# Performance work log

Hardware: AMD Instinct MI355X
Metric: run time of the kernel (lower is better)

The kernel has to match this reference:

```python
import jax, jax.numpy as jnp
import numpy as np

CH = [32, 64, 128, 256, 512]
# per decoder stage s (s=0 deepest): conv_a Cin = CH[3-s] + in_ch, Cout = CH[3-s]; conv_b CH[3-s]->CH[3-s]
STAGE_DIMS = [(768, 256), (384, 128), (192, 64), (96, 32)]


def three_interpolation(p1, p2, x2):
    """p1 [B,N1,3] dense coords, p2 [B,N2,3] sparse coords, x2 [B,C,N2] -> [B,C,N1]."""
    d2 = (jnp.sum(p1 * p1, -1)[:, :, None]
          - 2.0 * jnp.einsum('bnd,bmd->bnm', p1, p2)
          + jnp.sum(p2 * p2, -1)[:, None, :])            # [B,N1,N2] squared dists
    neg_d, idx = jax.lax.top_k(-d2, 3)                   # 3 nearest neighbors
    dist = jnp.maximum(-neg_d, 0.0)                      # [B,N1,3]
    w = 1.0 / (dist + 1e-8)
    w = w / jnp.sum(w, axis=-1, keepdims=True)           # inverse-distance weights
    gathered = jax.vmap(lambda x, i: x[:, i])(x2, idx)   # [B,C,N1,3]
    return jnp.einsum('bcnk,bnk->bcn', gathered, w)


def conv_bn_relu(x, W, g, b):
    # 1x1 conv1d + BN (eval: running mean 0, var 1) + ReLU
    y = jnp.einsum('oc,bcn->bon', W, x)
    return jax.nn.relu(y * g[None, :, None] + b[None, :, None])


def setup_inputs() -> dict:
    key = jax.random.key(0)
    B = 8
    Ns = [8192, 2048, 512, 128, 32]
    inp = {}
    keys = jax.random.split(key, 64)
    ki = 0
    for i, n in enumerate(Ns):
        inp[f'p{i}'] = jax.random.uniform(keys[ki], (B, n, 3), jnp.float32); ki += 1
        inp[f'f{i}'] = jax.random.normal(keys[ki], (B, CH[i], n), jnp.float32); ki += 1
    for s, (cin, cout) in enumerate(STAGE_DIMS):
        inp[f'w{s}a'] = jax.random.normal(keys[ki], (cout, cin), jnp.float32) * 0.05; ki += 1
        inp[f'g{s}a'] = 1.0 + 0.1 * jax.random.normal(keys[ki], (cout,), jnp.float32); ki += 1
        inp[f'b{s}a'] = 0.1 * jax.random.normal(keys[ki], (cout,), jnp.float32); ki += 1
        inp[f'w{s}b'] = jax.random.normal(keys[ki], (cout, cout), jnp.float32) * 0.05; ki += 1
        inp[f'g{s}b'] = 1.0 + 0.1 * jax.random.normal(keys[ki], (cout,), jnp.float32); ki += 1
        inp[f'b{s}b'] = 0.1 * jax.random.normal(keys[ki], (cout,), jnp.float32); ki += 1
    return inp


def reference(p0, p1, p2, p3, p4, f0, f1, f2, f3, f4,
              w0a, g0a, b0a, w0b, g0b, b0b,
              w1a, g1a, b1a, w1b, g1b, b1b,
              w2a, g2a, b2a, w2b, g2b, b2b,
              w3a, g3a, b3a, w3b, g3b, b3b):
    p = [p0, p1, p2, p3, p4]
    f = [f0, f1, f2, f3, f4]
    params = [(w0a, g0a, b0a, w0b, g0b, b0b),
              (w1a, g1a, b1a, w1b, g1b, b1b),
              (w2a, g2a, b2a, w2b, g2b, b2b),
              (w3a, g3a, b3a, w3b, g3b, b3b)]
    # decoder stage s propagates level (4-s) -> (3-s)
    for s in range(4):
        lvl = 3 - s
        interp = three_interpolation(p[lvl], p[lvl + 1], f[lvl + 1])
        x = jnp.concatenate([f[lvl], interp], axis=1)
        wa, ga, ba, wb, gb, bb = params[s]
        x = conv_bn_relu(x, wa, ga, ba)
        x = conv_bn_relu(x, wb, gb, bb)
        f[lvl] = x
    return f[0]
```

## Files before the change

kernel.cpp:

```cpp
#include <hip/hip_runtime.h>

#define KNN_INF 3.0e38f

struct KnnAll {
    const float* p1[4]; const float* p2[4];
    float* pd[4]; int* pi[4];
    int N1[4], N2[4], chunk[4], nchunk[4], nbx[4];
    int blkStart[4];
    int bs1, bs2, bs3;
};

__global__ void knn_all_kernel(KnnAll P) {
    __shared__ float4 sm4[256];
    int bid = blockIdx.x;
    int s = (bid >= P.bs1) + (bid >= P.bs2) + (bid >= P.bs3);
    int start = (s == 0) ? 0 : (s == 1) ? P.bs1 : (s == 2) ? P.bs2 : P.bs3;
    int local = bid - start;
    int nbx = P.nbx[s];
    int bx = local % nbx;
    int rest = local / nbx;
    int b = rest & 7;
    int z = rest >> 3;
    int N1 = P.N1[s], N2 = P.N2[s], chunk = P.chunk[s], nchunk = P.nchunk[s];
    int m0 = z * chunk;
    const float* p2b = P.p2[s] + ((size_t)b * N2 + m0) * 3;
    for (int m = threadIdx.x; m < chunk; m += blockDim.x) {
        float x = p2b[m * 3 + 0], y = p2b[m * 3 + 1], zz = p2b[m * 3 + 2];
        sm4[m] = make_float4(x, y, zz, x * x + y * y + zz * zz);
    }
    __syncthreads();
    int n = bx * blockDim.x + threadIdx.x;
    if (n >= N1) return;
    const float* p1b = P.p1[s] + ((size_t)b * N1 + n) * 3;
    float px = p1b[0], py = p1b[1], pz = p1b[2];
    float s1 = px * px + py * py + pz * pz;
    float d0 = KNN_INF, d1 = KNN_INF, d2 = KNN_INF;
    int i0 = 0, i1 = 0, i2 = 0;
    for (int m = 0; m < chunk; ++m) {
        float4 q = sm4[m];
        float dot = px * q.x + py * q.y + pz * q.z;
        float d = fmaf(-2.0f, dot, s1 + q.w);
        if (d < d2) {
            if (d < d1) {
                d2 = d1; i2 = i1;
                if (d < d0) { d1 = d0; i1 = i0; d0 = d; i0 = m; }
                else        { d1 = d;  i1 = m; }
            } else { d2 = d; i2 = m; }
        }
    }
    size_t base = (((size_t)b * N1 + n) * nchunk + z) * 3;
    float* pd = P.pd[s]; int* pi = P.pi[s];
    pd[base + 0] = d0; pd[base + 1] = d1; pd[base + 2] = d2;
    pi[base + 0] = m0 + i0; pi[base + 1] = m0 + i1; pi[base + 2] = m0 + i2;
}

struct MergeAll {
    const float* pd[4]; const int* pi[4];
    int* idx[4]; float* w[4];
    int nchunk[4], N1[4];
    int ts1, ts2, ts3;
};

__global__ void knn_merge_all_kernel(MergeAll P) {
    int t = blockIdx.x * blockDim.x + threadIdx.x;
    int s = (t >= P.ts1) + (t >= P.ts2) + (t >= P.ts3);
    int start = (s == 0) ? 0 : (s == 1) ? P.ts1 : (s == 2) ? P.ts2 : P.ts3;
    int lt = t - start;
    int nchunk = P.nchunk[s];
    float d0 = KNN_INF, d1 = KNN_INF, d2 = KNN_INF;
    int i0 = 0, i1 = 0, i2 = 0;
    const float* pd = P.pd[s]; const int* pi = P.pi[s];
    size_t base = (size_t)lt * nchunk * 3;
    for (int c = 0; c < nchunk * 3; ++c) {
        float d = pd[base + c];
        int   i = pi[base + c];
        if (d < d2) {
            if (d < d1) {
                d2 = d1; i2 = i1;
                if (d < d0) { d1 = d0; i1 = i0; d0 = d; i0 = i; }
                else        { d1 = d;  i1 = i; }
            } else { d2 = d; i2 = i; }
        }
    }
    float dd0 = fmaxf(d0, 0.0f), dd1 = fmaxf(d1, 0.0f), dd2 = fmaxf(d2, 0.0f);
    float w0 = 1.0f / (dd0 + 1e-8f);
    float w1 = 1.0f / (dd1 + 1e-8f);
    float w2 = 1.0f / (dd2 + 1e-8f);
    float wsum = w0 + w1 + w2;
    w0 /= wsum; w1 /= wsum; w2 /= wsum;
    size_t ob = (size_t)lt * 3;
    P.idx[s][ob + 0] = i0; P.idx[s][ob + 1] = i1; P.idx[s][ob + 2] = i2;
    P.w[s][ob + 0] = w0; P.w[s][ob + 1] = w1; P.w[s][ob + 2] = w2;
}

#define TO 32
#define TN 64
#define BK 16
template<bool PARTIAL>
__global__ __launch_bounds__(256) void conv_a_fused_kernel(
    const float* __restrict__ f1,
    const float* __restrict__ x2,
    const int*   __restrict__ idxS,
    const float* __restrict__ wS,
    const float* __restrict__ W,
    const float* __restrict__ g,
    const float* __restrict__ bv,
    float* __restrict__ Y,
    int C1, int C2, int N, int N2, int Cout, int chunk) {
    __shared__ float Ws[BK][TO];
    __shared__ float Xs[BK][TN];
    int Cin = C1 + C2;
    int zb = blockIdx.z;
    int b = zb & 7;
    int split = zb >> 3;
    int kBase = split * chunk;
    int oBase = blockIdx.y * TO;
    int nBase = blockIdx.x * TN;
    int tid = threadIdx.x;
    int tx = tid & 15;
    int ty = tid >> 4;
    int nn = tid & 63;
    int kk0 = tid >> 6;
    int n = nBase + nn;
    size_t gb = ((size_t)b * N + n) * 3;
    int j0 = idxS[gb + 0], j1 = idxS[gb + 1], j2 = idxS[gb + 2];
    float w0g = wS[gb + 0], w1g = wS[gb + 1], w2g = wS[gb + 2];
    const float* f1b = f1 + (size_t)b * C1 * N;
    const float* x2b = x2 + (size_t)b * C2 * N2;
    float acc[2][4] = {{0.f, 0.f, 0.f, 0.f}, {0.f, 0.f, 0.f, 0.f}};
    for (int k0 = kBase; k0 < kBase + chunk; k0 += BK) {
        for (int t = tid; t < TO * BK; t += 256) {
            int o = t / BK, kk = t % BK;
            Ws[kk][o] = W[(size_t)(oBase + o) * Cin + k0 + kk];
        }
#pragma unroll
        for (int i = 0; i < 4; ++i) {
            int kk = kk0 + i * 4;
            int k = k0 + kk;
            float v;
            if (k < C1) {
                v = f1b[(size_t)k * N + n];
            } else {
                const float* r = x2b + (size_t)(k - C1) * N2;
                v = r[j0] * w0g + r[j1] * w1g + r[j2] * w2g;
            }
            Xs[kk][nn] = v;
        }
        __syncthreads();
#pragma unroll
        for (int kk = 0; kk < BK; ++kk) {
            float w0 = Ws[kk][ty * 2 + 0];
            float w1 = Ws[kk][ty * 2 + 1];
            float4 xv = *reinterpret_cast<const float4*>(&Xs[kk][tx * 4]);
            acc[0][0] = fmaf(w0, xv.x, acc[0][0]);
            acc[0][1] = fmaf(w0, xv.y, acc[0][1]);
            acc[0][2] = fmaf(w0, xv.z, acc[0][2]);
            acc[0][3] = fmaf(w0, xv.w, acc[0][3]);
            acc[1][0] = fmaf(w1, xv.x, acc[1][0]);
            acc[1][1] = fmaf(w1, xv.y, acc[1][1]);
            acc[1][2] = fmaf(w1, xv.z, acc[1][2]);
            acc[1][3] = fmaf(w1, xv.w, acc[1][3]);
        }
        __syncthreads();
    }
#pragma unroll
    for (int r = 0; r < 2; ++r) {
        int o = oBase + ty * 2 + r;
        float4 st;
        if (PARTIAL) {
            st.x = acc[r][0]; st.y = acc[r][1]; st.z = acc[r][2]; st.w = acc[r][3];
            *reinterpret_cast<float4*>(&Y[((size_t)zb * Cout + o) * N + nBase + tx * 4]) = st;
        } else {
            float gg = g[o], bb = bv[o];
            st.x = fmaxf(fmaf(acc[r][0], gg, bb), 0.0f);
            st.y = fmaxf(fmaf(acc[r][1], gg, bb), 0.0f);
            st.z = fmaxf(fmaf(acc[r][2], gg, bb), 0.0f);
            st.w = fmaxf(fmaf(acc[r][3], gg, bb), 0.0f);
            *reinterpret_cast<float4*>(&Y[((size_t)b * Cout + o) * N + nBase + tx * 4]) = st;
        }
    }
}

template<bool PARTIAL>
__global__ __launch_bounds__(256) void conv_gemm_kernel(
    const float* __restrict__ X,
    const float* __restrict__ W,
    const float* __restrict__ g,
    const float* __restrict__ bv,
    float* __restrict__ Y,
    int Cin, int Cout, int N, int chunk) {
    __shared__ float Ws[BK][TO];
    __shared__ float Xs[BK][TN];
    int zb = blockIdx.z;
    int b = zb & 7;
    int split = zb >> 3;
    int kBase = split * chunk;
    int oBase = blockIdx.y * TO;
    int nBase = blockIdx.x * TN;
    int tid = threadIdx.x;
    int tx = tid & 15;
    int ty = tid >> 4;
    float acc[2][4] = {{0.f, 0.f, 0.f, 0.f}, {0.f, 0.f, 0.f, 0.f}};
    const float* Xb = X + (size_t)b * Cin * N;
    for (int k0 = kBase; k0 < kBase + chunk; k0 += BK) {
        for (int t = tid; t < TO * BK; t += 256) {
            int o = t / BK, kk = t % BK;
            Ws[kk][o] = W[(size_t)(oBase + o) * Cin + k0 + kk];
        }
        for (int t = tid; t < BK * TN; t += 256) {
            int kk = t / TN, nnn = t % TN;
            Xs[kk][nnn] = Xb[(size_t)(k0 + kk) * N + nBase + nnn];
        }
        __syncthreads();
#pragma unroll
        for (int kk = 0; kk < BK; ++kk) {
            float w0 = Ws[kk][ty * 2 + 0];
            float w1 = Ws[kk][ty * 2 + 1];
            float4 xv = *reinterpret_cast<const float4*>(&Xs[kk][tx * 4]);
            acc[0][0] = fmaf(w0, xv.x, acc[0][0]);
            acc[0][1] = fmaf(w0, xv.y, acc[0][1]);
            acc[0][2] = fmaf(w0, xv.z, acc[0][2]);
            acc[0][3] = fmaf(w0, xv.w, acc[0][3]);
            acc[1][0] = fmaf(w1, xv.x, acc[1][0]);
            acc[1][1] = fmaf(w1, xv.y, acc[1][1]);
            acc[1][2] = fmaf(w1, xv.z, acc[1][2]);
            acc[1][3] = fmaf(w1, xv.w, acc[1][3]);
        }
        __syncthreads();
    }
#pragma unroll
    for (int r = 0; r < 2; ++r) {
        int o = oBase + ty * 2 + r;
        float4 st;
        if (PARTIAL) {
            st.x = acc[r][0]; st.y = acc[r][1]; st.z = acc[r][2]; st.w = acc[r][3];
            *reinterpret_cast<float4*>(&Y[((size_t)zb * Cout + o) * N + nBase + tx * 4]) = st;
        } else {
            float gg = g[o], bb = bv[o];
            st.x = fmaxf(fmaf(acc[r][0], gg, bb), 0.0f);
            st.y = fmaxf(fmaf(acc[r][1], gg, bb), 0.0f);
            st.z = fmaxf(fmaf(acc[r][2], gg, bb), 0.0f);
            st.w = fmaxf(fmaf(acc[r][3], gg, bb), 0.0f);
            *reinterpret_cast<float4*>(&Y[((size_t)b * Cout + o) * N + nBase + tx * 4]) = st;
        }
    }
}

__global__ void reduce_bn_relu_kernel(const float* __restrict__ part,
                                      const float* __restrict__ g,
                                      const float* __restrict__ bv,
                                      float* __restrict__ Y,
                                      int Cout, int N, int total4, int nsplit, int stride4) {
    int t = blockIdx.x * blockDim.x + threadIdx.x;
    if (t >= total4) return;
    const float4* p4 = reinterpret_cast<const float4*>(part);
    float4 a = p4[t];
    for (int s = 1; s < nsplit; ++s) {
        float4 v = p4[t + (size_t)s * stride4];
        a.x += v.x; a.y += v.y; a.z += v.z; a.w += v.w;
    }
    int o = ((t * 4) / N) % Cout;
    float gg = g[o], bb = bv[o];
    float4 st;
    st.x = fmaxf(fmaf(a.x, gg, bb), 0.0f);
    st.y = fmaxf(fmaf(a.y, gg, bb), 0.0f);
    st.z = fmaxf(fmaf(a.z, gg, bb), 0.0f);
    st.w = fmaxf(fmaf(a.w, gg, bb), 0.0f);
    reinterpret_cast<float4*>(Y)[t] = st;
}

extern "C" void kernel_launch(void* const* d_in, const int* in_sizes, int n_in,
                              void* d_out, int out_size, void* d_ws, size_t ws_size,
                              hipStream_t stream) {
    const int B = 8;
    const int Ns[5]  = {8192, 2048, 512, 128, 32};
    const int CHs[5] = {32, 64, 128, 256, 512};

    const float* p[5];
    const float* f[5];
    for (int i = 0; i < 5; ++i) {
        p[i] = (const float*)d_in[2 * i];
        f[i] = (const float*)d_in[2 * i + 1];
    }

    int N1s[4], N2s[4], C1s[4], C2s[4];
    for (int s = 0; s < 4; ++s) {
        int lvl = 3 - s;
        N1s[s] = Ns[lvl]; N2s[s] = Ns[lvl + 1];
        C1s[s] = CHs[lvl];
        C2s[s] = (s == 0) ? CHs[4] : CHs[lvl + 1];
    }
    const int nchunks[4] = {1, 4, 8, 8};
    int chunks[4], nbxs[4];
    for (int s = 0; s < 4; ++s) {
        chunks[s] = N2s[s] / nchunks[s];
        nbxs[s] = (N1s[s] + 255) / 256;
    }

    float* ws = (float*)d_ws;
    int*   knn_idx = (int*)ws;
    float* knn_w   = ws + 262144;
    float* part_d  = ws + 524288;
    int*   part_i  = (int*)(ws + 2621440);
    float* bufA    = ws + 4718592;
    float* out0    = ws + 6815744;
    float* out1    = ws + 7077888;
    float* out2    = ws + 7602176;
    float* gpart   = ws + 8650752;
    float* outs[4] = {out0, out1, out2, (float*)d_out};

    int idxOff[4], pOff[4];
    {
        int a = 0, q = 0;
        for (int s = 0; s < 4; ++s) {
            idxOff[s] = a; a += B * N1s[s] * 3;
            pOff[s] = q;  q += B * N1s[s] * nchunks[s] * 3;
        }
    }

    KnnAll KP;
    int blk = 0;
    int bsArr[4];
    for (int s = 0; s < 4; ++s) {
        KP.p1[s] = p[3 - s]; KP.p2[s] = p[4 - s];
        KP.pd[s] = part_d + pOff[s]; KP.pi[s] = part_i + pOff[s];
        KP.N1[s] = N1s[s]; KP.N2[s] = N2s[s];
        KP.chunk[s] = chunks[s]; KP.nchunk[s] = nchunks[s]; KP.nbx[s] = nbxs[s];
        bsArr[s] = blk;
        blk += nbxs[s] * B * nchunks[s];
    }
    KP.bs1 = (blk, bsArr[1]); KP.bs2 = bsArr[2]; KP.bs3 = bsArr[3];
    knn_all_kernel<<<blk, 256, 0, stream>>>(KP);

    MergeAll MP;
    int tt = 0;
    int tsArr[4];
    for (int s = 0; s < 4; ++s) {
        MP.pd[s] = part_d + pOff[s]; MP.pi[s] = part_i + pOff[s];
        MP.idx[s] = knn_idx + idxOff[s]; MP.w[s] = knn_w + idxOff[s];
        MP.nchunk[s] = nchunks[s]; MP.N1[s] = N1s[s];
        tsArr[s] = tt;
        tt += B * N1s[s];
    }
    MP.ts1 = tsArr[1]; MP.ts2 = tsArr[2]; MP.ts3 = tsArr[3];
    knn_merge_all_kernel<<<(tt + 255) / 256, 256, 0, stream>>>(MP);

    const int nsA[4] = {6, 3, 2, 1};
    const int nsB[4] = {4, 2, 1, 1};

    for (int s = 0; s < 4; ++s) {
        int N1 = N1s[s], N2 = N2s[s];
        int C1 = C1s[s], C2 = C2s[s];
        int Cin = C1 + C2, Cout = C1;
        const float* x2 = (s == 0) ? f[4] : outs[s - 1];
        const float* wa = (const float*)d_in[10 + s * 6 + 0];
        const float* ga = (const float*)d_in[10 + s * 6 + 1];
        const float* ba = (const float*)d_in[10 + s * 6 + 2];
        const float* wb = (const float*)d_in[10 + s * 6 + 3];
        const float* gb = (const float*)d_in[10 + s * 6 + 4];
        const float* bb = (const float*)d_in[10 + s * 6 + 5];
        const int* idxS = knn_idx + idxOff[s];
        const float* wSb = knn_w + idxOff[s];

        {
            int nsplit = nsA[s];
            int chunk = Cin / nsplit;
            dim3 grid(N1 / TN, Cout / TO, B * nsplit);
            if (nsplit == 1) {
                conv_a_fused_kernel<false><<<grid, 256, 0, stream>>>(
                    f[3 - s], x2, idxS, wSb, wa, ga, ba, bufA, C1, C2, N1, N2, Cout, chunk);
            } else {
                conv_a_fused_kernel<true><<<grid, 256, 0, stream>>>(
                    f[3 - s], x2, idxS, wSb, wa, ga, ba, gpart, C1, C2, N1, N2, Cout, chunk);
                int total4 = B * Cout * N1 / 4;
                reduce_bn_relu_kernel<<<(total4 + 255) / 256, 256, 0, stream>>>(
                    gpart, ga, ba, bufA, Cout, N1, total4, nsplit, total4);
            }
        }
        {
            int nsplit = nsB[s];
            int chunk = Cout / nsplit;
            dim3 grid(N1 / TN, Cout / TO, B * nsplit);
            if (nsplit == 1) {
                conv_gemm_kernel<false><<<grid, 256, 0, stream>>>(
                    bufA, wb, gb, bb, outs[s], Cout, Cout, N1, chunk);
            } else {
                conv_gemm_kernel<true><<<grid, 256, 0, stream>>>(
                    bufA, wb, gb, bb, gpart, Cout, Cout, N1, chunk);
                int total4 = B * Cout * N1 / 4;
                reduce_bn_relu_kernel<<<(total4 + 255) / 256, 256, 0, stream>>>(
                    gpart, gb, bb, outs[s], Cout, N1, total4, nsplit, total4);
            }
        }
    }
}
```

Before: 231.5 us.

## Use uniform grid binning for last-stage KNN and increase split-K factors

Replaces the brute-force chunked 3-NN search for the largest stage (8192 queries vs 2048 points) with a per-batch uniform 8x8x8 grid: a binning kernel counting-sorts points into cells, and a query kernel scans neighbouring cells with an expanding ring and an early-exit bound. This removes most of the O(N1*N2) distance work and the partial/merge traffic for that stage. Ties are broken by original index to match top_k ordering. It also doubles the split-K factors for the conv GEMMs in the deeper stages to raise parallelism, at the cost of more partial-sum reduction traffic.

```diff
diff --git a/kernel.cpp b/kernel.cpp
--- a/kernel.cpp
+++ b/kernel.cpp
@@ -1,20 +1,163 @@
 #include <hip/hip_runtime.h>
 
 #define KNN_INF 3.0e38f
+#define GD 8
+#define NCELL 512
+#define H 0.125f
+
+
+__global__ __launch_bounds__(512) void bin_kernel(const float* __restrict__ p2,
+                                                  float4* __restrict__ bpts,
+                                                  int* __restrict__ bidx,
+                                                  int* __restrict__ cstart,
+                                                  int N2) {
+    __shared__ int cnt[NCELL], cnt0[NCELL], cur[NCELL];
+    __shared__ int cellof[2048];
+    int b = blockIdx.x;
+    int t = threadIdx.x;
+    cnt[t] = 0;
+    __syncthreads();
+    float xs[4], ys[4], zs[4];
+    for (int i = 0; i < 4; ++i) {
+        int m = t * 4 + i;
+        const float* q = p2 + ((size_t)b * N2 + m) * 3;
+        float x = q[0], y = q[1], z = q[2];
+        xs[i] = x; ys[i] = y; zs[i] = z;
+        int ix = min(GD - 1, max(0, (int)(x * 8.0f)));
+        int iy = min(GD - 1, max(0, (int)(y * 8.0f)));
+        int iz = min(GD - 1, max(0, (int)(z * 8.0f)));
+        int c = (ix << 6) | (iy << 3) | iz;
+        cellof[m] = c;
+        atomicAdd(&cnt[c], 1);
+    }
+    __syncthreads();
+    int myc = cnt[t];
+    cnt0[t] = myc;
+    __syncthreads();
+    for (int off = 1; off < NCELL; off <<= 1) {
+        int v = (t >= off) ? cnt[t - off] : 0;
+        __syncthreads();
+        cnt[t] += v;
+        __syncthreads();
+    }
+    int excl = cnt[t] - cnt0[t];
+    cur[t] = excl;
+    cstart[b * (NCELL + 1) + t] = excl;
+    if (t == 0) cstart[b * (NCELL + 1) + NCELL] = N2;
+    __syncthreads();
+    for (int i = 0; i < 4; ++i) {
+        int m = t * 4 + i;
+        int c = cellof[m];
+        int pos = atomicAdd(&cur[c], 1);
+        float x = xs[i], y = ys[i], z = zs[i];
+        bpts[(size_t)b * N2 + pos] = make_float4(x, y, z, x * x + y * y + z * z);
+        bidx[(size_t)b * N2 + pos] = m;
+    }
+}
+
+__device__ __forceinline__ bool lex_lt(float da, int ia, float db, int ib) {
+    return (da < db) || (da == db && ia < ib);
+}
+
+__global__ __launch_bounds__(256) void knn_query_kernel(
+    const float* __restrict__ p1,
+    const float4* __restrict__ bpts,
+    const int* __restrict__ bidx,
+    const int* __restrict__ cstart,
+    int* __restrict__ idx, float* __restrict__ w,
+    int N1, int N2) {
+    int n = blockIdx.x * 256 + threadIdx.x;
+    int b = blockIdx.y;
+    if (n >= N1) return;
+    const float* pp = p1 + ((size_t)b * N1 + n) * 3;
+    float px = pp[0], py = pp[1], pz = pp[2];
+    float s1 = px * px + py * py + pz * pz;
+    int cx = min(GD - 1, max(0, (int)(px * 8.0f)));
+    int cy = min(GD - 1, max(0, (int)(py * 8.0f)));
+    int cz = min(GD - 1, max(0, (int)(pz * 8.0f)));
+    float d0 = KNN_INF, d1 = KNN_INF, d2 = KNN_INF;
+    int i0 = 0, i1 = 0, i2 = 0;
+    const float4* bp = bpts + (size_t)b * N2;
+    const int* bi = bidx + (size_t)b * N2;
+    const int* cs = cstart + b * (NCELL + 1);
+
+#define SCAN_CELL(ci, cj, ck)                                            \
+    {                                                                    \
+        int c_ = ((ci) << 6) | ((cj) << 3) | (ck);                       \
+        int e_ = cs[c_ + 1];                                             \
+        for (int m_ = cs[c_]; m_ < e_; ++m_) {                           \
+            float4 q = bp[m_];                                           \
+            int om = bi[m_];                                             \
+            float dot = px * q.x + py * q.y + pz * q.z;                  \
+            float d = fmaf(-2.0f, dot, s1 + q.w);                        \
+            if (lex_lt(d, om, d2, i2)) {                                 \
+                if (lex_lt(d, om, d1, i1)) {                             \
+                    d2 = d1; i2 = i1;                                    \
+                    if (lex_lt(d, om, d0, i0)) {                         \
+                        d1 = d0; i1 = i0; d0 = d; i0 = om;               \
+                    } else { d1 = d; i1 = om; }                          \
+                } else { d2 = d; i2 = om; }                              \
+            }                                                            \
+        }                                                                \
+    }
+
+    int x0 = max(cx - 1, 0), x1 = min(cx + 1, GD - 1);
+    int y0 = max(cy - 1, 0), y1 = min(cy + 1, GD - 1);
+    int z0 = max(cz - 1, 0), z1 = min(cz + 1, GD - 1);
+    for (int i = x0; i <= x1; ++i)
+        for (int j = y0; j <= y1; ++j)
+            for (int k = z0; k <= z1; ++k)
+                SCAN_CELL(i, j, k);
+
+    int r = 1;
+    while (true) {
+        float mL = (cx - r > 0)      ? (px - (float)(cx - r) * H)     : KNN_INF;
+        float mR = (cx + r < GD - 1) ? ((float)(cx + r + 1) * H - px) : KNN_INF;
+        float mD = (cy - r > 0)      ? (py - (float)(cy - r) * H)     : KNN_INF;
+        float mU = (cy + r < GD - 1) ? ((float)(cy + r + 1) * H - py) : KNN_INF;
+        float mB = (cz - r > 0)      ? (pz - (float)(cz - r) * H)     : KNN_INF;
+        float mF = (cz + r < GD - 1) ? ((float)(cz + r + 1) * H - pz) : KNN_INF;
+        float mg = fminf(fminf(fminf(mL, mR), fminf(mD, mU)), fminf(mB, mF));
+        if (mg >= 1.0e18f) break;
+        if (d2 <= mg * mg * 0.99999f) break;
+        int nx0 = max(cx - r - 1, 0), nx1 = min(cx + r + 1, GD - 1);
+        int ny0 = max(cy - r - 1, 0), ny1 = min(cy + r + 1, GD - 1);
+        int nz0 = max(cz - r - 1, 0), nz1 = min(cz + r + 1, GD - 1);
+        for (int i = nx0; i <= nx1; ++i)
+            for (int j = ny0; j <= ny1; ++j)
+                for (int k = nz0; k <= nz1; ++k) {
+                    if (i >= x0 && i <= x1 && j >= y0 && j <= y1 && k >= z0 && k <= z1)
+                        continue;
+                    SCAN_CELL(i, j, k);
+                }
+        x0 = nx0; x1 = nx1; y0 = ny0; y1 = ny1; z0 = nz0; z1 = nz1;
+        ++r;
+    }
+#undef SCAN_CELL
+
+    float dd0 = fmaxf(d0, 0.0f), dd1 = fmaxf(d1, 0.0f), dd2 = fmaxf(d2, 0.0f);
+    float w0 = 1.0f / (dd0 + 1e-8f);
+    float w1 = 1.0f / (dd1 + 1e-8f);
+    float w2 = 1.0f / (dd2 + 1e-8f);
+    float wsum = w0 + w1 + w2;
+    w0 /= wsum; w1 /= wsum; w2 /= wsum;
+    size_t ob = ((size_t)b * N1 + n) * 3;
+    idx[ob + 0] = i0; idx[ob + 1] = i1; idx[ob + 2] = i2;
+    w[ob + 0] = w0; w[ob + 1] = w1; w[ob + 2] = w2;
+}
 
 struct KnnAll {
-    const float* p1[4]; const float* p2[4];
-    float* pd[4]; int* pi[4];
-    int N1[4], N2[4], chunk[4], nchunk[4], nbx[4];
-    int blkStart[4];
-    int bs1, bs2, bs3;
+    const float* p1[3]; const float* p2[3];
+    float* pd[3]; int* pi[3];
+    int N1[3], N2[3], chunk[3], nchunk[3], nbx[3];
+    int bs1, bs2;
 };
 
 __global__ void knn_all_kernel(KnnAll P) {
     __shared__ float4 sm4[256];
     int bid = blockIdx.x;
-    int s = (bid >= P.bs1) + (bid >= P.bs2) + (bid >= P.bs3);
-    int start = (s == 0) ? 0 : (s == 1) ? P.bs1 : (s == 2) ? P.bs2 : P.bs3;
+    int s = (bid >= P.bs1) + (bid >= P.bs2);
+    int start = (s == 0) ? 0 : (s == 1) ? P.bs1 : P.bs2;
     int local = bid - start;
     int nbx = P.nbx[s];
     int bx = local % nbx;
@@ -55,16 +198,17 @@
 }
 
 struct MergeAll {
-    const float* pd[4]; const int* pi[4];
-    int* idx[4]; float* w[4];
-    int nchunk[4], N1[4];
-    int ts1, ts2, ts3;
+    const float* pd[3]; const int* pi[3];
+    int* idx[3]; float* w[3];
+    int nchunk[3];
+    int ts1, ts2;
 };
 
-__global__ void knn_merge_all_kernel(MergeAll P) {
+__global__ void knn_merge_all_kernel(MergeAll P, int total) {
     int t = blockIdx.x * blockDim.x + threadIdx.x;
-    int s = (t >= P.ts1) + (t >= P.ts2) + (t >= P.ts3);
-    int start = (s == 0) ? 0 : (s == 1) ? P.ts1 : (s == 2) ? P.ts2 : P.ts3;
+    if (t >= total) return;
+    int s = (t >= P.ts1) + (t >= P.ts2);
+    int start = (s == 0) ? 0 : (s == 1) ? P.ts1 : P.ts2;
     int lt = t - start;
     int nchunk = P.nchunk[s];
     float d0 = KNN_INF, d1 = KNN_INF, d2 = KNN_INF;
@@ -98,13 +242,9 @@
 #define BK 16
 template<bool PARTIAL>
 __global__ __launch_bounds__(256) void conv_a_fused_kernel(
-    const float* __restrict__ f1,
-    const float* __restrict__ x2,
-    const int*   __restrict__ idxS,
-    const float* __restrict__ wS,
-    const float* __restrict__ W,
-    const float* __restrict__ g,
-    const float* __restrict__ bv,
+    const float* __restrict__ f1, const float* __restrict__ x2,
+    const int* __restrict__ idxS, const float* __restrict__ wS,
+    const float* __restrict__ W, const float* __restrict__ g, const float* __restrict__ bv,
     float* __restrict__ Y,
     int C1, int C2, int N, int N2, int Cout, int chunk) {
     __shared__ float Ws[BK][TO];
@@ -183,12 +323,9 @@
 
 template<bool PARTIAL>
 __global__ __launch_bounds__(256) void conv_gemm_kernel(
-    const float* __restrict__ X,
-    const float* __restrict__ W,
-    const float* __restrict__ g,
-    const float* __restrict__ bv,
-    float* __restrict__ Y,
-    int Cin, int Cout, int N, int chunk) {
+    const float* __restrict__ X, const float* __restrict__ W,
+    const float* __restrict__ g, const float* __restrict__ bv,
+    float* __restrict__ Y, int Cin, int Cout, int N, int chunk) {
     __shared__ float Ws[BK][TO];
     __shared__ float Xs[BK][TN];
     int zb = blockIdx.z;
@@ -290,9 +427,9 @@
         C1s[s] = CHs[lvl];
         C2s[s] = (s == 0) ? CHs[4] : CHs[lvl + 1];
     }
-    const int nchunks[4] = {1, 4, 8, 8};
-    int chunks[4], nbxs[4];
-    for (int s = 0; s < 4; ++s) {
+    const int nchunks[3] = {1, 4, 8};
+    int chunks[3], nbxs[3];
+    for (int s = 0; s < 3; ++s) {
         chunks[s] = N2s[s] / nchunks[s];
         nbxs[s] = (N1s[s] + 255) / 256;
     }
@@ -301,27 +438,37 @@
     int*   knn_idx = (int*)ws;
     float* knn_w   = ws + 262144;
     float* part_d  = ws + 524288;
-    int*   part_i  = (int*)(ws + 2621440);
-    float* bufA    = ws + 4718592;
-    float* out0    = ws + 6815744;
-    float* out1    = ws + 7077888;
-    float* out2    = ws + 7602176;
-    float* gpart   = ws + 8650752;
+    int*   part_i  = (int*)(ws + 969728);
+    float* bufA    = ws + 1415168;
+    float* out0    = ws + 3512320;
+    float* out1    = ws + 3774464;
+    float* out2    = ws + 4298752;
+    float* gpart   = ws + 5347328;
+    float4* bin_pts = (float4*)(ws + 9541632);
+    int*   bin_idx  = (int*)(ws + 9672704);
+    int*   cell_st  = (int*)(ws + 9689088);
     float* outs[4] = {out0, out1, out2, (float*)d_out};
 
-    int idxOff[4], pOff[4];
+    int idxOff[4], pOff[3];
     {
-        int a = 0, q = 0;
-        for (int s = 0; s < 4; ++s) {
-            idxOff[s] = a; a += B * N1s[s] * 3;
-            pOff[s] = q;  q += B * N1s[s] * nchunks[s] * 3;
-        }
+        int a = 0;
+        for (int s = 0; s < 4; ++s) { idxOff[s] = a; a += B * N1s[s] * 3; }
+        int q = 0;
+        for (int s = 0; s < 3; ++s) { pOff[s] = q; q += B * N1s[s] * nchunks[s] * 3; }
+    }
+
+    bin_kernel<<<B, 512, 0, stream>>>(p[1], bin_pts, bin_idx, cell_st, N2s[3]);
+    {
+        dim3 qg(N1s[3] / 256, B);
+        knn_query_kernel<<<qg, 256, 0, stream>>>(p[0], bin_pts, bin_idx, cell_st,
+                                                 knn_idx + idxOff[3], knn_w + idxOff[3],
+                                                 N1s[3], N2s[3]);
     }
 
     KnnAll KP;
     int blk = 0;
-    int bsArr[4];
-    for (int s = 0; s < 4; ++s) {
+    int bsArr[3];
+    for (int s = 0; s < 3; ++s) {
         KP.p1[s] = p[3 - s]; KP.p2[s] = p[4 - s];
         KP.pd[s] = part_d + pOff[s]; KP.pi[s] = part_i + pOff[s];
         KP.N1[s] = N1s[s]; KP.N2[s] = N2s[s];
@@ -329,24 +476,24 @@
         bsArr[s] = blk;
         blk += nbxs[s] * B * nchunks[s];
     }
-    KP.bs1 = (blk, bsArr[1]); KP.bs2 = bsArr[2]; KP.bs3 = bsArr[3];
+    KP.bs1 = bsArr[1]; KP.bs2 = bsArr[2];
     knn_all_kernel<<<blk, 256, 0, stream>>>(KP);
 
     MergeAll MP;
     int tt = 0;
-    int tsArr[4];
-    for (int s = 0; s < 4; ++s) {
+    int tsArr[3];
+    for (int s = 0; s < 3; ++s) {
         MP.pd[s] = part_d + pOff[s]; MP.pi[s] = part_i + pOff[s];
         MP.idx[s] = knn_idx + idxOff[s]; MP.w[s] = knn_w + idxOff[s];
-        MP.nchunk[s] = nchunks[s]; MP.N1[s] = N1s[s];
+        MP.nchunk[s] = nchunks[s];
         tsArr[s] = tt;
         tt += B * N1s[s];
     }
-    MP.ts1 = tsArr[1]; MP.ts2 = tsArr[2]; MP.ts3 = tsArr[3];
-    knn_merge_all_kernel<<<(tt + 255) / 256, 256, 0, stream>>>(MP);
-
-    const int nsA[4] = {6, 3, 2, 1};
-    const int nsB[4] = {4, 2, 1, 1};
+    MP.ts1 = tsArr[1]; MP.ts2 = tsArr[2];
+    knn_merge_all_kernel<<<(tt + 255) / 256, 256, 0, stream>>>(MP, tt);
+
+    const int nsA[4] = {12, 6, 4, 1};
+    const int nsB[4] = {8, 4, 2, 1};
 
     for (int s = 0; s < 4; ++s) {
         int N1 = N1s[s], N2 = N2s[s];
```

Result: slower. 271.5 us (+17.3%).

## Pre-pack sparse coords into float4 and read them directly in KNN scan

Applied to the files above, without the earlier changes.

Adds a pack kernel that converts the sparse point clouds into float4 (xyz plus squared norm) once. The KNN scan then reads these packed values straight from global memory (uniform, cached loads) instead of staging them in shared memory with a barrier. It also drops the per-point s1 add from the inner loop and adds it back only at the end. The merge kernel gains a bounds check and the workspace layout is reshuffled. This costs one extra launch and trades LDS reads for cached global reads in the hot loop.

```diff
diff --git a/kernel.cpp b/kernel.cpp
--- a/kernel.cpp
+++ b/kernel.cpp
@@ -2,16 +2,30 @@
 
 #define KNN_INF 3.0e38f
 
-struct KnnAll {
-    const float* p1[4]; const float* p2[4];
+struct PackAll {
+    const float* src[4];
+    float4* dst[4];
+    int c1, c2, c3;
+};
+__global__ void pack_kernel(PackAll P, int total) {
+    int t = blockIdx.x * 256 + threadIdx.x;
+    if (t >= total) return;
+    int s = (t >= P.c1) + (t >= P.c2) + (t >= P.c3);
+    int start = (s == 0) ? 0 : (s == 1) ? P.c1 : (s == 2) ? P.c2 : P.c3;
+    int i = t - start;
+    const float* q = P.src[s] + (size_t)i * 3;
+    float x = q[0], y = q[1], z = q[2];
+    P.dst[s][i] = make_float4(x, y, z, x * x + y * y + z * z);
+}
+
+struct KnnAll4 {
+    const float* p1[4];
+    const float4* c4[4];
     float* pd[4]; int* pi[4];
     int N1[4], N2[4], chunk[4], nchunk[4], nbx[4];
-    int blkStart[4];
     int bs1, bs2, bs3;
 };
-
-__global__ void knn_all_kernel(KnnAll P) {
-    __shared__ float4 sm4[256];
+__global__ __launch_bounds__(256) void knn_all_kernel(KnnAll4 P) {
     int bid = blockIdx.x;
     int s = (bid >= P.bs1) + (bid >= P.bs2) + (bid >= P.bs3);
     int start = (s == 0) ? 0 : (s == 1) ? P.bs1 : (s == 2) ? P.bs2 : P.bs3;
@@ -23,46 +37,41 @@
     int z = rest >> 3;
     int N1 = P.N1[s], N2 = P.N2[s], chunk = P.chunk[s], nchunk = P.nchunk[s];
     int m0 = z * chunk;
-    const float* p2b = P.p2[s] + ((size_t)b * N2 + m0) * 3;
-    for (int m = threadIdx.x; m < chunk; m += blockDim.x) {
-        float x = p2b[m * 3 + 0], y = p2b[m * 3 + 1], zz = p2b[m * 3 + 2];
-        sm4[m] = make_float4(x, y, zz, x * x + y * y + zz * zz);
-    }
-    __syncthreads();
-    int n = bx * blockDim.x + threadIdx.x;
+    const float4* __restrict__ cb = P.c4[s] + (size_t)b * N2 + m0;
+    int n = bx * 256 + threadIdx.x;
     if (n >= N1) return;
     const float* p1b = P.p1[s] + ((size_t)b * N1 + n) * 3;
     float px = p1b[0], py = p1b[1], pz = p1b[2];
     float s1 = px * px + py * py + pz * pz;
-    float d0 = KNN_INF, d1 = KNN_INF, d2 = KNN_INF;
+    float t0 = KNN_INF, t1 = KNN_INF, t2 = KNN_INF;
     int i0 = 0, i1 = 0, i2 = 0;
     for (int m = 0; m < chunk; ++m) {
-        float4 q = sm4[m];
+        float4 q = cb[m];
         float dot = px * q.x + py * q.y + pz * q.z;
-        float d = fmaf(-2.0f, dot, s1 + q.w);
-        if (d < d2) {
-            if (d < d1) {
-                d2 = d1; i2 = i1;
-                if (d < d0) { d1 = d0; i1 = i0; d0 = d; i0 = m; }
-                else        { d1 = d;  i1 = m; }
-            } else { d2 = d; i2 = m; }
+        float t = fmaf(-2.0f, dot, q.w);
+        if (t < t2) {
+            if (t < t1) {
+                t2 = t1; i2 = i1;
+                if (t < t0) { t1 = t0; i1 = i0; t0 = t; i0 = m; }
+                else        { t1 = t;  i1 = m; }
+            } else { t2 = t; i2 = m; }
         }
     }
     size_t base = (((size_t)b * N1 + n) * nchunk + z) * 3;
     float* pd = P.pd[s]; int* pi = P.pi[s];
-    pd[base + 0] = d0; pd[base + 1] = d1; pd[base + 2] = d2;
+    pd[base + 0] = s1 + t0; pd[base + 1] = s1 + t1; pd[base + 2] = s1 + t2;
     pi[base + 0] = m0 + i0; pi[base + 1] = m0 + i1; pi[base + 2] = m0 + i2;
 }
 
-struct MergeAll {
+struct MergeAll4 {
     const float* pd[4]; const int* pi[4];
     int* idx[4]; float* w[4];
-    int nchunk[4], N1[4];
+    int nchunk[4];
     int ts1, ts2, ts3;
 };
-
-__global__ void knn_merge_all_kernel(MergeAll P) {
+__global__ void knn_merge_all_kernel(MergeAll4 P, int total) {
     int t = blockIdx.x * blockDim.x + threadIdx.x;
+    if (t >= total) return;
     int s = (t >= P.ts1) + (t >= P.ts2) + (t >= P.ts3);
     int start = (s == 0) ? 0 : (s == 1) ? P.ts1 : (s == 2) ? P.ts2 : P.ts3;
     int lt = t - start;
@@ -98,13 +107,9 @@
 #define BK 16
 template<bool PARTIAL>
 __global__ __launch_bounds__(256) void conv_a_fused_kernel(
-    const float* __restrict__ f1,
-    const float* __restrict__ x2,
-    const int*   __restrict__ idxS,
-    const float* __restrict__ wS,
-    const float* __restrict__ W,
-    const float* __restrict__ g,
-    const float* __restrict__ bv,
+    const float* __restrict__ f1, const float* __restrict__ x2,
+    const int* __restrict__ idxS, const float* __restrict__ wS,
+    const float* __restrict__ W, const float* __restrict__ g, const float* __restrict__ bv,
     float* __restrict__ Y,
     int C1, int C2, int N, int N2, int Cout, int chunk) {
     __shared__ float Ws[BK][TO];
@@ -183,12 +188,9 @@
 
 template<bool PARTIAL>
 __global__ __launch_bounds__(256) void conv_gemm_kernel(
-    const float* __restrict__ X,
-    const float* __restrict__ W,
-    const float* __restrict__ g,
-    const float* __restrict__ bv,
-    float* __restrict__ Y,
-    int Cin, int Cout, int N, int chunk) {
+    const float* __restrict__ X, const float* __restrict__ W,
+    const float* __restrict__ g, const float* __restrict__ bv,
+    float* __restrict__ Y, int Cin, int Cout, int N, int chunk) {
     __shared__ float Ws[BK][TO];
     __shared__ float Xs[BK][TN];
     int zb = blockIdx.z;
@@ -301,49 +303,61 @@
     int*   knn_idx = (int*)ws;
     float* knn_w   = ws + 262144;
     float* part_d  = ws + 524288;
-    int*   part_i  = (int*)(ws + 2621440);
-    float* bufA    = ws + 4718592;
-    float* out0    = ws + 6815744;
-    float* out1    = ws + 7077888;
-    float* out2    = ws + 7602176;
-    float* gpart   = ws + 8650752;
+    int*   part_i  = (int*)(ws + 524288 + 2018304);
+    float* bufA    = ws + 524288;
+    float* gpart   = ws + 524288 + 2097152;
+    float* out0    = ws + 4718592;
+    float* out1    = ws + 4980736;
+    float* out2    = ws + 5505024;
+    float4* packed = (float4*)(ws + 6553600);
     float* outs[4] = {out0, out1, out2, (float*)d_out};
 
-    int idxOff[4], pOff[4];
+    int idxOff[4], pOff[4], pkOff[4];
     {
-        int a = 0, q = 0;
+        int a = 0, q = 0, k = 0;
         for (int s = 0; s < 4; ++s) {
             idxOff[s] = a; a += B * N1s[s] * 3;
             pOff[s] = q;  q += B * N1s[s] * nchunks[s] * 3;
-        }
-    }
-
-    KnnAll KP;
-    int blk = 0;
-    int bsArr[4];
-    for (int s = 0; s < 4; ++s) {
-        KP.p1[s] = p[3 - s]; KP.p2[s] = p[4 - s];
+            pkOff[s] = k; k += B * N2s[s];
+        }
+    }
+
+    PackAll PK;
+    int cum = 0, cArr[4];
+    for (int s = 0; s < 4; ++s) {
+        PK.src[s] = p[4 - s];
+        PK.dst[s] = packed + pkOff[s];
+        cArr[s] = cum;
+        cum += B * N2s[s];
+    }
+    PK.c1 = cArr[1]; PK.c2 = cArr[2]; PK.c3 = cArr[3];
+    pack_kernel<<<(cum + 255) / 256, 256, 0, stream>>>(PK, cum);
+
+    KnnAll4 KP;
+    int blk = 0, bsArr[4];
+    for (int s = 0; s < 4; ++s) {
+        KP.p1[s] = p[3 - s];
+        KP.c4[s] = packed + pkOff[s];
         KP.pd[s] = part_d + pOff[s]; KP.pi[s] = part_i + pOff[s];
         KP.N1[s] = N1s[s]; KP.N2[s] = N2s[s];
         KP.chunk[s] = chunks[s]; KP.nchunk[s] = nchunks[s]; KP.nbx[s] = nbxs[s];
         bsArr[s] = blk;
         blk += nbxs[s] * B * nchunks[s];
     }
-    KP.bs1 = (blk, bsArr[1]); KP.bs2 = bsArr[2]; KP.bs3 = bsArr[3];
+    KP.bs1 = bsArr[1]; KP.bs2 = bsArr[2]; KP.bs3 = bsArr[3];
     knn_all_kernel<<<blk, 256, 0, stream>>>(KP);
 
-    MergeAll MP;
-    int tt = 0;
-    int tsArr[4];
+    MergeAll4 MP;
+    int tt = 0, tsArr[4];
     for (int s = 0; s < 4; ++s) {
         MP.pd[s] = part_d + pOff[s]; MP.pi[s] = part_i + pOff[s];
         MP.idx[s] = knn_idx + idxOff[s]; MP.w[s] = knn_w + idxOff[s];
-        MP.nchunk[s] = nchunks[s]; MP.N1[s] = N1s[s];
+        MP.nchunk[s] = nchunks[s];
         tsArr[s] = tt;
         tt += B * N1s[s];
     }
     MP.ts1 = tsArr[1]; MP.ts2 = tsArr[2]; MP.ts3 = tsArr[3];
-    knn_merge_all_kernel<<<(tt + 255) / 256, 256, 0, stream>>>(MP);
+    knn_merge_all_kernel<<<(tt + 255) / 256, 256, 0, stream>>>(MP, tt);
 
     const int nsA[4] = {6, 3, 2, 1};
     const int nsB[4] = {4, 2, 1, 1};
```

Measured after the change: 247.7 us. +7.0%, slower.

## Fuse conv_a and conv_b into one kernel for the two shallow stages

Applied to the files above, without the earlier changes.

Adds a kernel that computes the interpolated concat, the first 1x1 conv with BN/ReLU kept in shared memory, and then the second 1x1 conv, all within one block. It is used for the stages with 64 and 32 output channels. This removes the intermediate bufA round trip to global memory and one launch per stage. The cost is fewer, larger blocks that hold all output channels per block, which reduces parallelism and adds shared-memory pressure. It also adds a bounds guard to the merge kernel and cleans up unused fields.

```diff
diff --git a/kernel.cpp b/kernel.cpp
--- a/kernel.cpp
+++ b/kernel.cpp
@@ -6,7 +6,6 @@
     const float* p1[4]; const float* p2[4];
     float* pd[4]; int* pi[4];
     int N1[4], N2[4], chunk[4], nchunk[4], nbx[4];
-    int blkStart[4];
     int bs1, bs2, bs3;
 };
 
@@ -57,12 +56,13 @@
 struct MergeAll {
     const float* pd[4]; const int* pi[4];
     int* idx[4]; float* w[4];
-    int nchunk[4], N1[4];
+    int nchunk[4];
     int ts1, ts2, ts3;
 };
 
-__global__ void knn_merge_all_kernel(MergeAll P) {
+__global__ void knn_merge_all_kernel(MergeAll P, int total) {
     int t = blockIdx.x * blockDim.x + threadIdx.x;
+    if (t >= total) return;
     int s = (t >= P.ts1) + (t >= P.ts2) + (t >= P.ts3);
     int start = (s == 0) ? 0 : (s == 1) ? P.ts1 : (s == 2) ? P.ts2 : P.ts3;
     int lt = t - start;
@@ -96,15 +96,12 @@
 #define TO 32
 #define TN 64
 #define BK 16
+
 template<bool PARTIAL>
 __global__ __launch_bounds__(256) void conv_a_fused_kernel(
-    const float* __restrict__ f1,
-    const float* __restrict__ x2,
-    const int*   __restrict__ idxS,
-    const float* __restrict__ wS,
-    const float* __restrict__ W,
-    const float* __restrict__ g,
-    const float* __restrict__ bv,
+    const float* __restrict__ f1, const float* __restrict__ x2,
+    const int* __restrict__ idxS, const float* __restrict__ wS,
+    const float* __restrict__ W, const float* __restrict__ g, const float* __restrict__ bv,
     float* __restrict__ Y,
     int C1, int C2, int N, int N2, int Cout, int chunk) {
     __shared__ float Ws[BK][TO];
@@ -183,12 +180,9 @@
 
 template<bool PARTIAL>
 __global__ __launch_bounds__(256) void conv_gemm_kernel(
-    const float* __restrict__ X,
-    const float* __restrict__ W,
-    const float* __restrict__ g,
-    const float* __restrict__ bv,
-    float* __restrict__ Y,
-    int Cin, int Cout, int N, int chunk) {
+    const float* __restrict__ X, const float* __restrict__ W,
+    const float* __restrict__ g, const float* __restrict__ bv,
+    float* __restrict__ Y, int Cin, int Cout, int N, int chunk) {
     __shared__ float Ws[BK][TO];
     __shared__ float Xs[BK][TN];
     int zb = blockIdx.z;
@@ -269,6 +263,116 @@
     reinterpret_cast<float4*>(Y)[t] = st;
 }
 
+template<int COUT, int TNF>
+__global__ __launch_bounds__(256) void conv_ab_fused_kernel(
+    const float* __restrict__ f1, const float* __restrict__ x2,
+    const int* __restrict__ idxS, const float* __restrict__ wS,
+    const float* __restrict__ Wa, const float* __restrict__ ga, const float* __restrict__ ba,
+    const float* __restrict__ Wb, const float* __restrict__ gbv, const float* __restrict__ bbv,
+    float* __restrict__ Y,
+    int C1, int C2, int N, int N2) {
+    constexpr int TX  = TNF / 4;
+    constexpr int RPP = 256 / TNF;
+    __shared__ float Ws_[BK][COUT];
+    __shared__ float Xs[BK][TNF];
+    __shared__ float Ya[COUT][TNF];
+    int Cin = C1 + C2;
+    int b = blockIdx.z;
+    int nBase = blockIdx.x * TNF;
+    int tid = threadIdx.x;
+    int tx = tid % TX;
+    int ty = tid / TX;
+    int nn = tid % TNF;
+    int kk0 = tid / TNF;
+    int n = nBase + nn;
+    size_t gb = ((size_t)b * N + n) * 3;
+    int j0 = idxS[gb + 0], j1 = idxS[gb + 1], j2 = idxS[gb + 2];
+    float w0g = wS[gb + 0], w1g = wS[gb + 1], w2g = wS[gb + 2];
+    const float* f1b = f1 + (size_t)b * C1 * N;
+    const float* x2b = x2 + (size_t)b * C2 * N2;
+    float acc[2][4] = {{0.f, 0.f, 0.f, 0.f}, {0.f, 0.f, 0.f, 0.f}};
+    for (int k0 = 0; k0 < Cin; k0 += BK) {
+        for (int t = tid; t < COUT * BK; t += 256) {
+            int o = t / BK, kk = t % BK;
+            Ws_[kk][o] = Wa[(size_t)o * Cin + k0 + kk];
+        }
+#pragma unroll
+        for (int i = 0; i < BK / RPP; ++i) {
+            int kk = kk0 + i * RPP;
+            int k = k0 + kk;
+            float v;
+            if (k < C1) {
+                v = f1b[(size_t)k * N + n];
+            } else {
+                const float* r = x2b + (size_t)(k - C1) * N2;
+                v = r[j0] * w0g + r[j1] * w1g + r[j2] * w2g;
+            }
+            Xs[kk][nn] = v;
+        }
+        __syncthreads();
+#pragma unroll
+        for (int kk = 0; kk < BK; ++kk) {
+            float w0 = Ws_[kk][ty * 2 + 0];
+            float w1 = Ws_[kk][ty * 2 + 1];
+            float4 xv = *reinterpret_cast<const float4*>(&Xs[kk][tx * 4]);
+            acc[0][0] = fmaf(w0, xv.x, acc[0][0]);
+            acc[0][1] = fmaf(w0, xv.y, acc[0][1]);
+            acc[0][2] = fmaf(w0, xv.z, acc[0][2]);
+            acc[0][3] = fmaf(w0, xv.w, acc[0][3]);
+            acc[1][0] = fmaf(w1, xv.x, acc[1][0]);
+            acc[1][1] = fmaf(w1, xv.y, acc[1][1]);
+            acc[1][2] = fmaf(w1, xv.z, acc[1][2]);
+            acc[1][3] = fmaf(w1, xv.w, acc[1][3]);
+        }
+        __syncthreads();
+    }
+#pragma unroll
+    for (int r = 0; r < 2; ++r) {
+        int o = ty * 2 + r;
+        float gg = ga[o], bb = ba[o];
+        float4 st;
+        st.x = fmaxf(fmaf(acc[r][0], gg, bb), 0.0f);
+        st.y = fmaxf(fmaf(acc[r][1], gg, bb), 0.0f);
+        st.z = fmaxf(fmaf(acc[r][2], gg, bb), 0.0f);
+        st.w = fmaxf(fmaf(acc[r][3], gg, bb), 0.0f);
+        *reinterpret_cast<float4*>(&Ya[o][tx * 4]) = st;
+        acc[r][0] = acc[r][1] = acc[r][2] = acc[r][3] = 0.f;
+    }
+    for (int k0 = 0; k0 < COUT; k0 += BK) {
+        __syncthreads();
+        for (int t = tid; t < COUT * BK; t += 256) {
+            int o = t / BK, kk = t % BK;
+            Ws_[kk][o] = Wb[(size_t)o * COUT + k0 + kk];
+        }
+        __syncthreads();
+#pragma unroll
+        for (int kk = 0; kk < BK; ++kk) {
+            float w0 = Ws_[kk][ty * 2 + 0];
+            float w1 = Ws_[kk][ty * 2 + 1];
+            float4 xv = *reinterpret_cast<const float4*>(&Ya[k0 + kk][tx * 4]);
+            acc[0][0] = fmaf(w0, xv.x, acc[0][0]);
+            acc[0][1] = fmaf(w0, xv.y, acc[0][1]);
+            acc[0][2] = fmaf(w0, xv.z, acc[0][2]);
+            acc[0][3] = fmaf(w0, xv.w, acc[0][3]);
+            acc[1][0] = fmaf(w1, xv.x, acc[1][0]);
+            acc[1][1] = fmaf(w1, xv.y, acc[1][1]);
+            acc[1][2] = fmaf(w1, xv.z, acc[1][2]);
+            acc[1][3] = fmaf(w1, xv.w, acc[1][3]);
+        }
+    }
+#pragma unroll
+    for (int r = 0; r < 2; ++r) {
+        int o = ty * 2 + r;
+        float gg = gbv[o], bb = bbv[o];
+        float4 st;
+        st.x = fmaxf(fmaf(acc[r][0], gg, bb), 0.0f);
+        st.y = fmaxf(fmaf(acc[r][1], gg, bb), 0.0f);
+        st.z = fmaxf(fmaf(acc[r][2], gg, bb), 0.0f);
+        st.w = fmaxf(fmaf(acc[r][3], gg, bb), 0.0f);
+        *reinterpret_cast<float4*>(&Y[((size_t)b * COUT + o) * N + nBase + tx * 4]) = st;
+    }
+}
+
 extern "C" void kernel_launch(void* const* d_in, const int* in_sizes, int n_in,
                               void* d_out, int out_size, void* d_ws, size_t ws_size,
                               hipStream_t stream) {
@@ -319,8 +423,7 @@
     }
 
     KnnAll KP;
-    int blk = 0;
-    int bsArr[4];
+    int blk = 0, bsArr[4];
     for (int s = 0; s < 4; ++s) {
         KP.p1[s] = p[3 - s]; KP.p2[s] = p[4 - s];
         KP.pd[s] = part_d + pOff[s]; KP.pi[s] = part_i + pOff[s];
@@ -329,21 +432,20 @@
         bsArr[s] = blk;
         blk += nbxs[s] * B * nchunks[s];
     }
-    KP.bs1 = (blk, bsArr[1]); KP.bs2 = bsArr[2]; KP.bs3 = bsArr[3];
+    KP.bs1 = bsArr[1]; KP.bs2 = bsArr[2]; KP.bs3 = bsArr[3];
     knn_all_kernel<<<blk, 256, 0, stream>>>(KP);
 
     MergeAll MP;
-    int tt = 0;
-    int tsArr[4];
+    int tt = 0, tsArr[4];
     for (int s = 0; s < 4; ++s) {
         MP.pd[s] = part_d + pOff[s]; MP.pi[s] = part_i + pOff[s];
         MP.idx[s] = knn_idx + idxOff[s]; MP.w[s] = knn_w + idxOff[s];
-        MP.nchunk[s] = nchunks[s]; MP.N1[s] = N1s[s];
+        MP.nchunk[s] = nchunks[s];
         tsArr[s] = tt;
         tt += B * N1s[s];
     }
     MP.ts1 = tsArr[1]; MP.ts2 = tsArr[2]; MP.ts3 = tsArr[3];
-    knn_merge_all_kernel<<<(tt + 255) / 256, 256, 0, stream>>>(MP);
+    knn_merge_all_kernel<<<(tt + 255) / 256, 256, 0, stream>>>(MP, tt);
 
     const int nsA[4] = {6, 3, 2, 1};
     const int nsB[4] = {4, 2, 1, 1};
@@ -362,35 +464,38 @@
         const int* idxS = knn_idx + idxOff[s];
         const float* wSb = knn_w + idxOff[s];
 
+        if (s == 2) {
+            dim3 grid(N1 / 32, 1, B);
+            conv_ab_fused_kernel<64, 32><<<grid, 256, 0, stream>>>(
+                f[3 - s], x2, idxS, wSb, wa, ga, ba, wb, gb, bb, outs[s], C1, C2, N1, N2);
+            continue;
+        }
+        if (s == 3) {
+            dim3 grid(N1 / 64, 1, B);
+            conv_ab_fused_kernel<32, 64><<<grid, 256, 0, stream>>>(
+                f[3 - s], x2, idxS, wSb, wa, ga, ba, wb, gb, bb, outs[s], C1, C2, N1, N2);
+            continue;
+        }
+
         {
             int nsplit = nsA[s];
             int chunk = Cin / nsplit;
             dim3 grid(N1 / TN, Cout / TO, B * nsplit);
-            if (nsplit == 1) {
-                conv_a_fused_kernel<false><<<grid, 256, 0, stream>>>(
-                    f[3 - s], x2, idxS, wSb, wa, ga, ba, bufA, C1, C2, N1, N2, Cout, chunk);
-            } else {
-                conv_a_fused_kernel<true><<<grid, 256, 0, stream>>>(
-                    f[3 - s], x2, idxS, wSb, wa, ga, ba, gpart, C1, C2, N1, N2, Cout, chunk);
-                int total4 = B * Cout * N1 / 4;
-                reduce_bn_relu_kernel<<<(total4 + 255) / 256, 256, 0, stream>>>(
-                    gpart, ga, ba, bufA, Cout, N1, total4, nsplit, total4);
-            }
+            conv_a_fused_kernel<true><<<grid, 256, 0, stream>>>(
+                f[3 - s], x2, idxS, wSb, wa, ga, ba, gpart, C1, C2, N1, N2, Cout, chunk);
+            int total4 = B * Cout * N1 / 4;
+            reduce_bn_relu_kernel<<<(total4 + 255) / 256, 256, 0, stream>>>(
+                gpart, ga, ba, bufA, Cout, N1, total4, nsplit, total4);
         }
         {
             int nsplit = nsB[s];
             int chunk = Cout / nsplit;
             dim3 grid(N1 / TN, Cout / TO, B * nsplit);
-            if (nsplit == 1) {
-                conv_gemm_kernel<false><<<grid, 256, 0, stream>>>(
-                    bufA, wb, gb, bb, outs[s], Cout, Cout, N1, chunk);
-            } else {
-                conv_gemm_kernel<true><<<grid, 256, 0, stream>>>(
-                    bufA, wb, gb, bb, gpart, Cout, Cout, N1, chunk);
-                int total4 = B * Cout * N1 / 4;
-                reduce_bn_relu_kernel<<<(total4 + 255) / 256, 256, 0, stream>>>(
-                    gpart, gb, bb, outs[s], Cout, N1, total4, nsplit, total4);
-            }
-        }
-    }
-}
+            conv_gemm_kernel<true><<<grid, 256, 0, stream>>>(
+                bufA, wb, gb, bb, gpart, Cout, Cout, N1, chunk);
+            int total4 = B * Cout * N1 / 4;
+            reduce_bn_relu_kernel<<<(total4 + 255) / 256, 256, 0, stream>>>(
+                gpart, gb, bb, outs[s], Cout, N1, total4, nsplit, total4);
+        }
+    }
+}
```

Result: slower. 242.2 us (+4.7%).
